# Performance work log

Hardware: AMD Instinct MI355X
Metric: run time of the kernel (lower is better)

## Reference

```python
import jax, jax.numpy as jnp
import numpy as np
import math

B, S, D, H = 4, 2048, 1024, 16
DH = D // H


def _make_random_mask(key, seq_length):
    # Vectorized equivalent of create_random_mask: keep exactly seq_length//2
    # uniformly-random positions per row.
    scores = jax.random.uniform(key, (seq_length, seq_length))
    kth = jax.lax.top_k(scores, seq_length // 2)[0][:, -1:]  # per-row threshold
    return scores >= kth  # bool [S, S], exactly S//2 True per row


def setup_inputs() -> dict:
    key = jax.random.key(0)
    ks = jax.random.split(key, 10)
    s = 1.0 / math.sqrt(D)
    return {
        "hidden_states": jax.random.normal(ks[0], (B, S, D), jnp.float32),
        "mask": _make_random_mask(ks[1], S),
        "Wq": jax.random.normal(ks[2], (D, D), jnp.float32) * s,
        "bq": jnp.zeros((D,), jnp.float32),
        "Wk": jax.random.normal(ks[3], (D, D), jnp.float32) * s,
        "bk": jnp.zeros((D,), jnp.float32),
        "Wv": jax.random.normal(ks[4], (D, D), jnp.float32) * s,
        "bv": jnp.zeros((D,), jnp.float32),
        "Wo": jax.random.normal(ks[5], (D, D), jnp.float32) * s,
        "bo": jnp.zeros((D,), jnp.float32),
    }


def reference(hidden_states, mask, Wq, bq, Wk, bk, Wv, bv, Wo, bo):
    b, s, d = hidden_states.shape
    scale = 1.0 / math.sqrt(DH)

    def heads(x):  # [B,S,D] -> [B,H,S,DH]
        return x.reshape(b, s, H, DH).transpose(0, 2, 1, 3)

    q = heads(hidden_states @ Wq + bq)
    k = heads(hidden_states @ Wk + bk)
    v = heads(hidden_states @ Wv + bv)

    scores = jnp.einsum("bhqd,bhkd->bhqk", q, k) * scale
    scores = jnp.where(mask[None, None], scores, jnp.float32(-1e9))
    probs = jax.nn.softmax(scores, axis=-1)  # attn_dropout rate = 0 (eval)

    ctx = jnp.einsum("bhqk,bhkd->bhqd", probs, v)
    ctx = ctx.transpose(0, 2, 1, 3).reshape(b, s, d)
    return ctx @ Wo + bo  # proj_dropout rate = 0 (eval); vis=False -> weights None
```

## Files before the change

kernel.cpp:

```cpp
#include <hip/hip_runtime.h>

typedef unsigned short u16;
typedef unsigned int   u32;
typedef unsigned long long u64;
typedef unsigned char  u8;
typedef __attribute__((ext_vector_type(8))) short bf16x8;
typedef __attribute__((ext_vector_type(4))) float f32x4;

#define B_  4
#define S_  2048
#define D_  1024
#define H_  16
#define DH_ 64

#define MFMA16 __builtin_amdgcn_mfma_f32_16x16x32_bf16

__device__ __forceinline__ u16 f2bf(float f) {
  u32 u = __builtin_bit_cast(u32, f);
  u32 r = (u + 0x7FFFu + ((u >> 16) & 1u)) >> 16;
  return (u16)r;
}

__device__ __forceinline__ u32 cvt_pk_bf16(float lo, float hi) {
  u32 r;
  asm("v_cvt_pk_bf16_f32 %0, %1, %2" : "=v"(r) : "v"(lo), "v"(hi));
  return r;
}

__device__ __forceinline__ float exp2_fast(float x) {
  float r;
  asm("v_exp_f32 %0, %1" : "=v"(r) : "v"(x));
  return r;
}

__device__ __forceinline__ void gload_lds16(const void* g, void* l) {
  __builtin_amdgcn_global_load_lds(
      (const __attribute__((address_space(1))) u32*)g,
      (__attribute__((address_space(3))) u32*)l,
      16, 0, 0);
}

__device__ __forceinline__ bf16x8 lds_frag(const u16* base, int row, int cb) {
  return *(const bf16x8*)((const char*)base + row * 128 + (cb ^ ((row & 7) << 4)));
}

__global__ __launch_bounds__(256) void prep(
    const float* __restrict__ x, u16* __restrict__ xb,
    const int* __restrict__ m, u64* __restrict__ mbw,
    const float* __restrict__ bq, const float* __restrict__ bk,
    const float* __restrict__ bv, float* __restrict__ fb) {
  const int blk = blockIdx.x;
  if (blk < 8192) {
    const int i = (blk * 256 + threadIdx.x) * 4;
    float4 v = *(const float4*)(x + i);
    ushort4 o;
    o.x = f2bf(v.x); o.y = f2bf(v.y); o.z = f2bf(v.z); o.w = f2bf(v.w);
    *(ushort4*)(xb + i) = o;
  } else if (blk < 8192 + 2048) {
    const int base = (blk - 8192) * 2048;
#pragma unroll
    for (int it = 0; it < 8; it++) {
      const int i = base + it * 256 + threadIdx.x;
      const u64 bits = __ballot(m[i] != 0);
      if ((threadIdx.x & 63) == 0) mbw[i >> 6] = bits;
    }
  } else {
    const int i = (blk - 10240) * 256 + threadIdx.x;
    fb[i] = i < 1024 ? bq[i] : (i < 2048 ? bk[i - 1024] : bv[i - 2048]);
  }
}

__global__ __launch_bounds__(256) void transpose_w(
    const float* __restrict__ W0, const float* __restrict__ W1,
    const float* __restrict__ W2, const float* __restrict__ W3,
    u16* __restrict__ T0, u16* __restrict__ T1,
    u16* __restrict__ T2, u16* __restrict__ T3) {
  __shared__ float t[64][65];
  const int z = blockIdx.z;
  const float* W = z == 0 ? W0 : z == 1 ? W1 : z == 2 ? W2 : W3;
  u16* T        = z == 0 ? T0 : z == 1 ? T1 : z == 2 ? T2 : T3;
  const int n0 = blockIdx.x * 64, k0 = blockIdx.y * 64;
  const int c = threadIdx.x & 63, r0 = threadIdx.x >> 6;
#pragma unroll
  for (int i = 0; i < 16; i++)
    t[r0 + i * 4][c] = W[(size_t)(k0 + r0 + i * 4) * 1024 + n0 + c];
  __syncthreads();
#pragma unroll
  for (int i = 0; i < 16; i++)
    T[(size_t)(n0 + r0 + i * 4) * 1024 + k0 + c] = f2bf(t[c][r0 + i * 4]);
}

__global__ __launch_bounds__(256) void gemm_bt(
    const u16* __restrict__ A, const u16* __restrict__ Bw,
    const float* __restrict__ bias, void* __restrict__ outp, int mode) {
  __shared__ u16 As[2][128 * 32];
  __shared__ u16 Bs[2][128 * 32];
  const int tid = threadIdx.x;
  const int lane = tid & 63, wid = tid >> 6;
  const int wr = wid >> 1, wc = wid & 1;
  const int bm = blockIdx.x, bn = blockIdx.y;
  const int lr = lane & 15, lk8 = (lane >> 4) * 8, lg = (lane >> 4) * 4;

  f32x4 acc[4][4];
#pragma unroll
  for (int i = 0; i < 4; i++)
#pragma unroll
    for (int j = 0; j < 4; j++) acc[i][j] = (f32x4){0.f, 0.f, 0.f, 0.f};

  const int r0 = tid >> 2;
  const int c0 = (tid & 3) * 8;
  const u16* gA = A + ((size_t)(bm * 128 + r0) << 10) + c0;
  const u16* gB = Bw + ((size_t)(bn * 128 + r0) << 10) + c0;

#define GSTAGE(ki, bf) do {                                        \
    const int kt_ = (ki) * 32;                                     \
    gload_lds16(gA + kt_, &As[bf][tid * 8]);                       \
    gload_lds16(gA + kt_ + (64 << 10), &As[bf][tid * 8 + 64 * 32]);\
    gload_lds16(gB + kt_, &Bs[bf][tid * 8]);                       \
    gload_lds16(gB + kt_ + (64 << 10), &Bs[bf][tid * 8 + 64 * 32]);\
  } while (0)

  GSTAGE(0, 0);
  __syncthreads();

  for (int ki = 0; ki < 32; ki++) {
    const int cur = ki & 1;
    if (ki + 1 < 32) GSTAGE(ki + 1, cur ^ 1);

    bf16x8 af[4], bfr[4];
#pragma unroll
    for (int mr = 0; mr < 4; mr++)
      af[mr] = *(const bf16x8*)&As[cur][(wr * 64 + mr * 16 + lr) * 32 + lk8];
#pragma unroll
    for (int nr = 0; nr < 4; nr++)
      bfr[nr] = *(const bf16x8*)&Bs[cur][(wc * 64 + nr * 16 + lr) * 32 + lk8];
    __builtin_amdgcn_s_setprio(1);
#pragma unroll
    for (int mr = 0; mr < 4; mr++)
#pragma unroll
      for (int nr = 0; nr < 4; nr++)
        acc[mr][nr] = MFMA16(af[mr], bfr[nr], acc[mr][nr], 0, 0, 0);
    __builtin_amdgcn_s_setprio(0);
    __syncthreads();
  }

#pragma unroll
  for (int mr = 0; mr < 4; mr++) {
#pragma unroll
    for (int nr = 0; nr < 4; nr++) {
      const int n = bn * 128 + wc * 64 + nr * 16 + lr;
      const float bv = bias[n];
#pragma unroll
      for (int r = 0; r < 4; r++) {
        const int m = bm * 128 + wr * 64 + mr * 16 + lg + r;
        float v = acc[mr][nr][r] + bv;
        if (mode == 2) {
          ((float*)outp)[(size_t)m * 1024 + n] = v;
        } else {
          const int which = n >> 10, col = n & 1023;
          const int bb = m >> 11, s = m & (S_ - 1);
          const int hh = col >> 6, dh = col & (DH_ - 1);
          if (which == 0) v *= 0.180336880f;
          u16* o = (u16*)outp + ((size_t)which << 23);
          if (which <= 1)
            o[((((size_t)bb * H_ + hh) * S_ + s) << 6) + dh] = f2bf(v);
          else
            o[(((size_t)(bb * H_ + hh) * DH_ + dh) << 11) + s] = f2bf(v);
        }
      }
    }
  }
}

__global__ __launch_bounds__(256) void attn(
    const u16* __restrict__ Q, const u16* __restrict__ K,
    const u16* __restrict__ Vt, const u64* __restrict__ mb,
    u16* __restrict__ ctx) {
  __shared__ u16 Kl[2][64 * 64];
  __shared__ u16 Vl[2][64 * 64];
  __shared__ u16 Pl[4][16 * 64];

  const int tid = threadIdx.x, lane = tid & 63, wid = tid >> 6;
  const int q0 = blockIdx.x * 64;
  const int h = blockIdx.y, b = blockIdx.z;
  const size_t bh = (size_t)b * H_ + h;
  const u16* Qb = Q + (bh * S_ << 6);
  const u16* Kb = K + (bh * S_ << 6);
  const u16* Vb = Vt + (bh * DH_ << 11);
  const int qh = lane & 15, g = lane >> 4, lk8 = g * 8;
  const int qrow = q0 + wid * 16 + qh;

  const bf16x8 qf0 = *(const bf16x8*)(Qb + ((size_t)qrow << 6) + lk8);
  const bf16x8 qf1 = *(const bf16x8*)(Qb + ((size_t)qrow << 6) + 32 + lk8);

  f32x4 acc[4];
#pragma unroll
  for (int i = 0; i < 4; i++) acc[i] = (f32x4){0.f, 0.f, 0.f, 0.f};
  float mrun = -1e30f, lrun = 0.f;

  const int sr = tid >> 3;
  const int scz = ((((tid & 7) * 16) ^ ((sr & 7) << 4)) >> 1);

#define ASTAGE(t, bf) do {                                                  \
    const int kt_ = (t) * 64;                                               \
    gload_lds16(Kb + ((size_t)(kt_ + sr) << 6) + scz, &Kl[bf][tid * 8]);    \
    gload_lds16(Kb + ((size_t)(kt_ + sr + 32) << 6) + scz,                  \
                &Kl[bf][tid * 8 + 32 * 64]);                                \
    gload_lds16(Vb + ((size_t)sr << 11) + kt_ + scz, &Vl[bf][tid * 8]);     \
    gload_lds16(Vb + ((size_t)(sr + 32) << 11) + kt_ + scz,                 \
                &Vl[bf][tid * 8 + 32 * 64]);                                \
  } while (0)

  ASTAGE(0, 0);
  __syncthreads();

  for (int t = 0; t < S_ / 64; t++) {
    const int cur = t & 1;
    if (t + 1 < S_ / 64) ASTAGE(t + 1, cur ^ 1);
    const u64 mw = mb[((size_t)qrow << 5) + t];

    f32x4 sc[4];
    __builtin_amdgcn_s_setprio(1);
#pragma unroll
    for (int nr = 0; nr < 4; nr++) {
      const int row = nr * 16 + qh;
      const bf16x8 kf0 = lds_frag(Kl[cur], row, lk8 * 2);
      const bf16x8 kf1 = lds_frag(Kl[cur], row, 64 + lk8 * 2);
      f32x4 z = (f32x4){0.f, 0.f, 0.f, 0.f};
      z = MFMA16(kf0, qf0, z, 0, 0, 0);
      z = MFMA16(kf1, qf1, z, 0, 0, 0);
      sc[nr] = z;
    }
    __builtin_amdgcn_s_setprio(0);

    const u64 mwg = mw >> (g * 4);
    const u32 mlo = (u32)mwg, mhi = (u32)(mwg >> 32);
#pragma unroll
    for (int nr = 0; nr < 4; nr++) {
      const u32 wsel = (nr & 2) ? mhi : mlo;
      const int sh = (nr & 1) * 16;
#pragma unroll
      for (int r = 0; r < 4; r++)
        if (!((wsel >> (sh + r)) & 1u)) sc[nr][r] = -1e9f;
    }

    float tmax = sc[0][0];
#pragma unroll
    for (int nr = 0; nr < 4; nr++)
#pragma unroll
      for (int r = 0; r < 4; r++) tmax = fmaxf(tmax, sc[nr][r]);
    tmax = fmaxf(tmax, __shfl_xor(tmax, 16));
    tmax = fmaxf(tmax, __shfl_xor(tmax, 32));

    if (!__all(tmax <= mrun + 8.0f)) {
      const float mnew = fmaxf(mrun, tmax);
      const float alpha = exp2_fast(mrun - mnew);
      lrun *= alpha;
      mrun = mnew;
#pragma unroll
      for (int r = 0; r < 4; r++) {
        const float as = __shfl(alpha, g * 4 + r);
        acc[0][r] *= as; acc[1][r] *= as; acc[2][r] *= as; acc[3][r] *= as;
      }
    }

    float ts = 0.f;
    u32 w[8];
#pragma unroll
    for (int nr = 0; nr < 4; nr++) {
      float p0 = exp2_fast(sc[nr][0] - mrun);
      float p1 = exp2_fast(sc[nr][1] - mrun);
      float p2 = exp2_fast(sc[nr][2] - mrun);
      float p3 = exp2_fast(sc[nr][3] - mrun);
      ts += (p0 + p1) + (p2 + p3);
      w[nr * 2]     = cvt_pk_bf16(p0, p1);
      w[nr * 2 + 1] = cvt_pk_bf16(p2, p3);
    }
    ts += __shfl_xor(ts, 16);
    ts += __shfl_xor(ts, 32);
    lrun += ts;

    {
      char* pw = (char*)Pl[wid] + qh * 128;
      const int sw = (qh & 7) << 4;
#pragma unroll
      for (int nr = 0; nr < 4; nr++) {
        *(u32*)(pw + ((g * 8 + nr * 32) ^ sw))     = w[nr * 2];
        *(u32*)(pw + ((g * 8 + 4 + nr * 32) ^ sw)) = w[nr * 2 + 1];
      }
    }

#pragma unroll
    for (int ks = 0; ks < 2; ks++) {
      const bf16x8 pf = lds_frag(Pl[wid], qh, ks * 64 + lk8 * 2);
      __builtin_amdgcn_s_setprio(1);
#pragma unroll
      for (int nc = 0; nc < 4; nc++) {
        const bf16x8 vf = lds_frag(Vl[cur], nc * 16 + qh, ks * 64 + lk8 * 2);
        acc[nc] = MFMA16(pf, vf, acc[nc], 0, 0, 0);
      }
      __builtin_amdgcn_s_setprio(0);
    }
    __syncthreads();
  }

  float linv[4];
#pragma unroll
  for (int r = 0; r < 4; r++) linv[r] = 1.0f / __shfl(lrun, g * 4 + r);
#pragma unroll
  for (int nc = 0; nc < 4; nc++)
#pragma unroll
    for (int r = 0; r < 4; r++) {
      const float o = acc[nc][r] * linv[r];
      const int ql = q0 + wid * 16 + g * 4 + r;
      ctx[((size_t)b * S_ + ql) * D_ + h * DH_ + nc * 16 + qh] = f2bf(o);
    }
}

extern "C" void kernel_launch(void* const* d_in, const int* in_sizes, int n_in,
                              void* d_out, int out_size, void* d_ws, size_t ws_size,
                              hipStream_t stream) {
  const float* X  = (const float*)d_in[0];
  const int* mask = (const int*)d_in[1];
  const float* Wq = (const float*)d_in[2];
  const float* bq = (const float*)d_in[3];
  const float* Wk = (const float*)d_in[4];
  const float* bk = (const float*)d_in[5];
  const float* Wv = (const float*)d_in[6];
  const float* bv = (const float*)d_in[7];
  const float* Wo = (const float*)d_in[8];
  const float* bo = (const float*)d_in[9];

  char* ws = (char*)d_ws;
  const size_t MB = 1024 * 1024;
  u16* xb  = (u16*)(ws);
  u16* q   = (u16*)(ws + 16 * MB);
  u16* wqt = (u16*)(ws + 64 * MB);
  u16* wkt = (u16*)(ws + 66 * MB);
  u16* wvt = (u16*)(ws + 68 * MB);
  u16* wot = (u16*)(ws + 70 * MB);
  u64* mbb = (u64*)(ws + 72 * MB);
  float* fb = (float*)(ws + 72 * MB + 512 * 1024);

  prep<<<10252, 256, 0, stream>>>(X, xb, mask, mbb, bq, bk, bv, fb);
  transpose_w<<<dim3(16, 16, 4), 256, 0, stream>>>(Wq, Wk, Wv, Wo, wqt, wkt, wvt, wot);

  gemm_bt<<<dim3(64, 24), 256, 0, stream>>>(xb, wqt, fb, q, 3);

  u16* k  = q + (1u << 23);
  u16* vt = q + (2u << 23);
  attn<<<dim3(S_ / 64, H_, B_), 256, 0, stream>>>(q, k, vt, mbb, xb);

  gemm_bt<<<dim3(64, 8), 256, 0, stream>>>(xb, wot, bo, d_out, 2);
}
```

Measured before the change: 363.8 us.

## Relax load barriers with vmcnt waits, remap blocks per XCD, streamline softmax masking

```diff
diff --git a/kernel.cpp b/kernel.cpp
--- a/kernel.cpp
+++ b/kernel.cpp
@@ -14,6 +14,11 @@
 #define DH_ 64
 
 #define MFMA16 __builtin_amdgcn_mfma_f32_16x16x32_bf16
+
+#define WAITV(NSTR) do {                                   \
+    asm volatile("s_waitcnt vmcnt(" NSTR ")" ::: "memory");\
+    __builtin_amdgcn_sched_barrier(0);                     \
+  } while (0)
 
 __device__ __forceinline__ u16 f2bf(float f) {
   u32 u = __builtin_bit_cast(u32, f);
@@ -92,13 +97,15 @@
 
 __global__ __launch_bounds__(256) void gemm_bt(
     const u16* __restrict__ A, const u16* __restrict__ Bw,
-    const float* __restrict__ bias, void* __restrict__ outp, int mode) {
+    const float* __restrict__ bias, void* __restrict__ outp,
+    int mode, int chunk) {
   __shared__ u16 As[2][128 * 32];
   __shared__ u16 Bs[2][128 * 32];
   const int tid = threadIdx.x;
   const int lane = tid & 63, wid = tid >> 6;
   const int wr = wid >> 1, wc = wid & 1;
-  const int bm = blockIdx.x, bn = blockIdx.y;
+  const int sid = (blockIdx.x & 7) * chunk + (blockIdx.x >> 3);
+  const int bm = sid & 63, bn = sid >> 6;
   const int lr = lane & 15, lk8 = (lane >> 4) * 8, lg = (lane >> 4) * 4;
 
   f32x4 acc[4][4];
@@ -121,11 +128,18 @@
   } while (0)
 
   GSTAGE(0, 0);
-  __syncthreads();
 
   for (int ki = 0; ki < 32; ki++) {
     const int cur = ki & 1;
-    if (ki + 1 < 32) GSTAGE(ki + 1, cur ^ 1);
+    __builtin_amdgcn_sched_barrier(0);
+    if (ki + 1 < 32) {
+      GSTAGE(ki + 1, cur ^ 1);
+      WAITV("4");
+    } else {
+      WAITV("0");
+    }
+    __builtin_amdgcn_s_barrier();
+    __builtin_amdgcn_sched_barrier(0);
 
     bf16x8 af[4], bfr[4];
 #pragma unroll
@@ -141,7 +155,7 @@
       for (int nr = 0; nr < 4; nr++)
         acc[mr][nr] = MFMA16(af[mr], bfr[nr], acc[mr][nr], 0, 0, 0);
     __builtin_amdgcn_s_setprio(0);
-    __syncthreads();
+    __builtin_amdgcn_s_barrier();
   }
 
 #pragma unroll
@@ -181,8 +195,9 @@
   __shared__ u16 Pl[4][16 * 64];
 
   const int tid = threadIdx.x, lane = tid & 63, wid = tid >> 6;
-  const int q0 = blockIdx.x * 64;
-  const int h = blockIdx.y, b = blockIdx.z;
+  const int sid = (blockIdx.x & 7) * 256 + (blockIdx.x >> 3);
+  const int q0 = (sid & 31) * 64;
+  const int h = (sid >> 5) & 15, b = sid >> 9;
   const size_t bh = (size_t)b * H_ + h;
   const u16* Qb = Q + (bh * S_ << 6);
   const u16* Kb = K + (bh * S_ << 6);
@@ -196,7 +211,7 @@
   f32x4 acc[4];
 #pragma unroll
   for (int i = 0; i < 4; i++) acc[i] = (f32x4){0.f, 0.f, 0.f, 0.f};
-  float mrun = -1e30f, lrun = 0.f;
+  float mrun = -1e30f, lsum = 0.f;
 
   const int sr = tid >> 3;
   const int scz = ((((tid & 7) * 16) ^ ((sr & 7) << 4)) >> 1);
@@ -212,11 +227,19 @@
   } while (0)
 
   ASTAGE(0, 0);
-  __syncthreads();
 
   for (int t = 0; t < S_ / 64; t++) {
     const int cur = t & 1;
-    if (t + 1 < S_ / 64) ASTAGE(t + 1, cur ^ 1);
+    __builtin_amdgcn_sched_barrier(0);
+    if (t + 1 < S_ / 64) {
+      ASTAGE(t + 1, cur ^ 1);
+      WAITV("4");
+    } else {
+      WAITV("0");
+    }
+    __builtin_amdgcn_s_barrier();
+    __builtin_amdgcn_sched_barrier(0);
+
     const u64 mw = mb[((size_t)qrow << 5) + t];
 
     f32x4 sc[4];
@@ -233,29 +256,19 @@
     }
     __builtin_amdgcn_s_setprio(0);
 
-    const u64 mwg = mw >> (g * 4);
-    const u32 mlo = (u32)mwg, mhi = (u32)(mwg >> 32);
-#pragma unroll
-    for (int nr = 0; nr < 4; nr++) {
-      const u32 wsel = (nr & 2) ? mhi : mlo;
-      const int sh = (nr & 1) * 16;
-#pragma unroll
-      for (int r = 0; r < 4; r++)
-        if (!((wsel >> (sh + r)) & 1u)) sc[nr][r] = -1e9f;
-    }
-
-    float tmax = sc[0][0];
-#pragma unroll
-    for (int nr = 0; nr < 4; nr++)
-#pragma unroll
-      for (int r = 0; r < 4; r++) tmax = fmaxf(tmax, sc[nr][r]);
-    tmax = fmaxf(tmax, __shfl_xor(tmax, 16));
-    tmax = fmaxf(tmax, __shfl_xor(tmax, 32));
+    float tmax = fmaxf(fmaxf(sc[0][0], sc[0][1]), sc[0][2]);
+    tmax = fmaxf(fmaxf(tmax, sc[0][3]), fmaxf(sc[1][0], sc[1][1]));
+    tmax = fmaxf(fmaxf(tmax, sc[1][2]), fmaxf(sc[1][3], sc[2][0]));
+    tmax = fmaxf(fmaxf(tmax, sc[2][1]), fmaxf(sc[2][2], sc[2][3]));
+    tmax = fmaxf(fmaxf(tmax, sc[3][0]), fmaxf(sc[3][1], sc[3][2]));
+    tmax = fmaxf(tmax, sc[3][3]);
 
     if (!__all(tmax <= mrun + 8.0f)) {
-      const float mnew = fmaxf(mrun, tmax);
+      float tq = fmaxf(tmax, __shfl_xor(tmax, 16));
+      tq = fmaxf(tq, __shfl_xor(tq, 32));
+      const float mnew = fmaxf(mrun, tq);
       const float alpha = exp2_fast(mrun - mnew);
-      lrun *= alpha;
+      lsum *= alpha;
       mrun = mnew;
 #pragma unroll
       for (int r = 0; r < 4; r++) {
@@ -264,21 +277,27 @@
       }
     }
 
+    const u64 mwg = mw >> (g * 4);
+    const u32 mlo = (u32)mwg, mhi = (u32)(mwg >> 32);
     float ts = 0.f;
     u32 w[8];
 #pragma unroll
     for (int nr = 0; nr < 4; nr++) {
+      const u32 wsel = (nr & 2) ? mhi : mlo;
+      const int sh = (nr & 1) * 16;
       float p0 = exp2_fast(sc[nr][0] - mrun);
       float p1 = exp2_fast(sc[nr][1] - mrun);
       float p2 = exp2_fast(sc[nr][2] - mrun);
       float p3 = exp2_fast(sc[nr][3] - mrun);
+      p0 = ((wsel >> (sh + 0)) & 1u) ? p0 : 0.f;
+      p1 = ((wsel >> (sh + 1)) & 1u) ? p1 : 0.f;
+      p2 = ((wsel >> (sh + 2)) & 1u) ? p2 : 0.f;
+      p3 = ((wsel >> (sh + 3)) & 1u) ? p3 : 0.f;
       ts += (p0 + p1) + (p2 + p3);
       w[nr * 2]     = cvt_pk_bf16(p0, p1);
       w[nr * 2 + 1] = cvt_pk_bf16(p2, p3);
     }
-    ts += __shfl_xor(ts, 16);
-    ts += __shfl_xor(ts, 32);
-    lrun += ts;
+    lsum += ts;
 
     {
       char* pw = (char*)Pl[wid] + qh * 128;
@@ -301,12 +320,14 @@
       }
       __builtin_amdgcn_s_setprio(0);
     }
-    __syncthreads();
+    __builtin_amdgcn_s_barrier();
   }
 
+  float lt = lsum + __shfl_xor(lsum, 16);
+  lt += __shfl_xor(lt, 32);
   float linv[4];
 #pragma unroll
-  for (int r = 0; r < 4; r++) linv[r] = 1.0f / __shfl(lrun, g * 4 + r);
+  for (int r = 0; r < 4; r++) linv[r] = 1.0f / __shfl(lt, g * 4 + r);
 #pragma unroll
   for (int nc = 0; nc < 4; nc++)
 #pragma unroll
@@ -345,11 +366,11 @@
   prep<<<10252, 256, 0, stream>>>(X, xb, mask, mbb, bq, bk, bv, fb);
   transpose_w<<<dim3(16, 16, 4), 256, 0, stream>>>(Wq, Wk, Wv, Wo, wqt, wkt, wvt, wot);
 
-  gemm_bt<<<dim3(64, 24), 256, 0, stream>>>(xb, wqt, fb, q, 3);
+  gemm_bt<<<1536, 256, 0, stream>>>(xb, wqt, fb, q, 3, 192);
 
   u16* k  = q + (1u << 23);
   u16* vt = q + (2u << 23);
-  attn<<<dim3(S_ / 64, H_, B_), 256, 0, stream>>>(q, k, vt, mbb, xb);
-
-  gemm_bt<<<dim3(64, 8), 256, 0, stream>>>(xb, wot, bo, d_out, 2);
-}
+  attn<<<2048, 256, 0, stream>>>(q, k, vt, mbb, xb);
+
+  gemm_bt<<<512, 256, 0, stream>>>(xb, wot, bo, d_out, 2, 64);
+}
```

Result: slower. 384.3 us (+5.6%).
